# Optimization experiments

Measured on AMD Instinct MI355X. Metric: run time of the kernel, lower is better.

## Reference

```python
import jax, jax.numpy as jnp
import numpy as np

B, C, H, W = 16, 128, 64, 64
C_OUT = 256
N_BANDS = 4
KS = [3, 5, 7, 11]
BN_EPS = 1e-5


def setup_inputs() -> dict:
    key = jax.random.key(0)
    ks = jax.random.split(key, 16)
    inp = {
        'x': jax.random.normal(ks[0], (B, C, H, W), dtype=jnp.float32),
        'conv_w0': jax.random.normal(ks[1], (C, 1, 3), dtype=jnp.float32) * 0.2,
        'conv_w1': jax.random.normal(ks[2], (C, 1, 5), dtype=jnp.float32) * 0.2,
        'conv_w2': jax.random.normal(ks[3], (C, 1, 7), dtype=jnp.float32) * 0.2,
        'conv_w3': jax.random.normal(ks[4], (C, 1, 11), dtype=jnp.float32) * 0.2,
        'bn_gamma': jax.random.uniform(ks[5], (N_BANDS, C), dtype=jnp.float32, minval=0.5, maxval=1.5),
        'bn_beta': jax.random.normal(ks[6], (N_BANDS, C), dtype=jnp.float32) * 0.1,
        'bn_mean': jax.random.normal(ks[7], (N_BANDS, C), dtype=jnp.float32) * 0.1,
        'bn_var': jax.random.uniform(ks[8], (N_BANDS, C), dtype=jnp.float32, minval=0.5, maxval=1.5),
        'scale_weights': jnp.ones((N_BANDS,), dtype=jnp.float32),
        'alpha': jnp.float32(0.5),
        'proj_w': jax.random.normal(ks[9], (C_OUT, C * N_BANDS), dtype=jnp.float32) * 0.04,
        'proj_b': jax.random.normal(ks[10], (C_OUT,), dtype=jnp.float32) * 0.02,
    }
    return inp


def _dwconv1d(xc, w):
    # xc: [B, C, L], w: [C, 1, k] depthwise, 'same' padding for odd k
    k = w.shape[-1]
    return jax.lax.conv_general_dilated(
        xc, w, window_strides=(1,), padding=[(k // 2, k // 2)],
        feature_group_count=xc.shape[1], dimension_numbers=('NCH', 'OIH', 'NCH'))


def _forward(x, conv_w0, conv_w1, conv_w2, conv_w3, bn_gamma, bn_beta, bn_mean,
             bn_var, scale_weights, alpha, proj_w, proj_b):
    b, c, h, w = x.shape
    L = h * w
    xs = x.reshape(b, c, L)                      # [B, C, L] (== x.view.transpose.transpose)
    norm_w = jax.nn.softmax(scale_weights)       # [n_bands]

    # --- multi-scale depthwise conv branch: conv -> BN(eval) -> GELU -> scale ---
    conv_bands = []
    for i, cw in enumerate([conv_w0, conv_w1, conv_w2, conv_w3]):
        y = _dwconv1d(xs, cw)                    # [B, C, L]
        inv = jax.lax.rsqrt(bn_var[i] + BN_EPS)  # [C]
        y = (y - bn_mean[i][:, None]) * (inv * bn_gamma[i])[:, None] + bn_beta[i][:, None]
        y = jax.nn.gelu(y, approximate=False)    # exact erf GELU (torch default)
        conv_bands.append(y.transpose(0, 2, 1) * norm_w[i])  # [B, L, C]

    # --- frequency band branch (interpolate to size L is identity: conv keeps L) ---
    xt = xs.transpose(0, 2, 1)                   # [B, L, C]
    Xf = jnp.fft.rfft(xt, axis=1)                # [B, n_freqs, C]
    n_freqs = L // 2 + 1
    band_size = n_freqs // N_BANDS
    fidx = jnp.arange(n_freqs)
    alpha_s = jax.nn.sigmoid(alpha)
    fused = []
    for i in range(N_BANDS):
        start = i * band_size
        end = (i + 1) * band_size if i < N_BANDS - 1 else n_freqs
        mask = (fidx >= start) & (fidx < end)
        band = jnp.fft.irfft(jnp.where(mask[None, :, None], Xf, 0), n=L, axis=1)
        fused.append(alpha_s * conv_bands[i] + (1.0 - alpha_s) * band)

    cat = jnp.concatenate(fused, axis=-1)        # [B, L, n_bands*C]
    out = cat @ proj_w.T + proj_b                # [B, L, C_out]
    return out.transpose(0, 2, 1).reshape(b, -1, h, w)


def reference(x, conv_w0, conv_w1, conv_w2, conv_w3, bn_gamma, bn_beta, bn_mean,
              bn_var, scale_weights, alpha, proj_w, proj_b):
    return _forward(x, conv_w0, conv_w1, conv_w2, conv_w3, bn_gamma, bn_beta,
                    bn_mean, bn_var, scale_weights, alpha, proj_w, proj_b)
```

## Files before the change

### kernel.cpp

```cpp
#include <hip/hip_runtime.h>
#include <math.h>

constexpr int LEN = 4096;
constexpr int NTHREADS = 512;
constexpr int PELEM = LEN / NTHREADS;
constexpr float INVN = 1.0f / 4096.0f;

typedef __attribute__((ext_vector_type(8))) short bf16x8;
typedef __attribute__((ext_vector_type(4))) float f32x4;

#define APHYS(I) ((I) + ((I) >> 5))
#define TPHYS(I) ((I) + ((I) >> 5))
#define ZOFF 8

__device__ __forceinline__ unsigned short f2bf(float f) {
    unsigned u = __float_as_uint(f);
    unsigned r = (u + 0x7fffu + ((u >> 16) & 1u)) >> 16;
    return (unsigned short)r;
}

__device__ __forceinline__ int digitrev4(int j) {
    int r = 0;
#pragma unroll
    for (int d = 0; d < 6; ++d) { r = (r << 2) | (j & 3); j >>= 2; }
    return r;
}

__device__ __forceinline__ void cmul(float ar, float ai, float br, float bi,
                                     float& cr, float& ci) {
    cr = ar * br - ai * bi;
    ci = ar * bi + ai * br;
}

template <bool CONJ>
__device__ __forceinline__ void loadtw3(const float* __restrict__ twr,
                                        const float* __restrict__ twi, int k1,
                                        float& w1r, float& w1i, float& w2r, float& w2i,
                                        float& w3r, float& w3i) {
    w1r = twr[TPHYS(k1)];
    float s = twi[TPHYS(k1)];
    w1i = CONJ ? -s : s;
    cmul(w1r, w1i, w1r, w1i, w2r, w2i);
    cmul(w1r, w1i, w2r, w2i, w3r, w3i);
}

__device__ void dif_fft(float* __restrict__ ar, float* __restrict__ ai,
                        const float* __restrict__ twr, const float* __restrict__ twi,
                        int tid) {
#pragma unroll
    for (int s = 5; s >= 0; --s) {
        __syncthreads();
        const int qshift = 2 * s;
        const int quarter = 1 << qshift;
        const int tshift = 2 * (5 - s);
#pragma unroll
        for (int u = 0; u < 1024 / NTHREADS; ++u) {
            int t = tid + NTHREADS * u;
            int j = t & (quarter - 1);
            int g = t >> qshift;
            int base = (g << (qshift + 2)) + j;
            int i0 = APHYS(base), i1 = APHYS(base + quarter),
                i2 = APHYS(base + 2 * quarter), i3 = APHYS(base + 3 * quarter);
            float x0r = ar[i0], x0i = ai[i0];
            float x1r = ar[i1], x1i = ai[i1];
            float x2r = ar[i2], x2i = ai[i2];
            float x3r = ar[i3], x3i = ai[i3];
            float t0r = x0r + x2r, t0i = x0i + x2i;
            float t1r = x0r - x2r, t1i = x0i - x2i;
            float t2r = x1r + x3r, t2i = x1i + x3i;
            float t3r = x1r - x3r, t3i = x1i - x3i;
            float y0r = t0r + t2r, y0i = t0i + t2i;
            float y2r = t0r - t2r, y2i = t0i - t2i;
            float y1r = t1r + t3i, y1i = t1i - t3r;
            float y3r = t1r - t3i, y3i = t1i + t3r;
            int k1 = j << tshift;
            float w1r, w1i, w2r, w2i, w3r, w3i;
            loadtw3<false>(twr, twi, k1, w1r, w1i, w2r, w2i, w3r, w3i);
            ar[i0] = y0r;                         ai[i0] = y0i;
            ar[i1] = y1r * w1r - y1i * w1i;       ai[i1] = y1r * w1i + y1i * w1r;
            ar[i2] = y2r * w2r - y2i * w2i;       ai[i2] = y2r * w2i + y2i * w2r;
            ar[i3] = y3r * w3r - y3i * w3i;       ai[i3] = y3r * w3i + y3i * w3r;
        }
    }
    __syncthreads();
}

__device__ void dit_ifft(float* __restrict__ ar, float* __restrict__ ai,
                         const float* __restrict__ twr, const float* __restrict__ twi,
                         int tid) {
#pragma unroll
    for (int s = 0; s <= 5; ++s) {
        __syncthreads();
        const int qshift = 2 * s;
        const int quarter = 1 << qshift;
        const int tshift = 2 * (5 - s);
#pragma unroll
        for (int u = 0; u < 1024 / NTHREADS; ++u) {
            int t = tid + NTHREADS * u;
            int j = t & (quarter - 1);
            int g = t >> qshift;
            int base = (g << (qshift + 2)) + j;
            int i0 = APHYS(base), i1 = APHYS(base + quarter),
                i2 = APHYS(base + 2 * quarter), i3 = APHYS(base + 3 * quarter);
            int k1 = j << tshift;
            float w1r, w1i, w2r, w2i, w3r, w3i;
            loadtw3<true>(twr, twi, k1, w1r, w1i, w2r, w2i, w3r, w3i);
            float x0r = ar[i0], x0i = ai[i0];
            float b1r = ar[i1], b1i = ai[i1];
            float b2r = ar[i2], b2i = ai[i2];
            float b3r = ar[i3], b3i = ai[i3];
            float x1r = b1r * w1r - b1i * w1i, x1i = b1r * w1i + b1i * w1r;
            float x2r = b2r * w2r - b2i * w2i, x2i = b2r * w2i + b2i * w2r;
            float x3r = b3r * w3r - b3i * w3i, x3i = b3r * w3i + b3i * w3r;
            float t0r = x0r + x2r, t0i = x0i + x2i;
            float t1r = x0r - x2r, t1i = x0i - x2i;
            float t2r = x1r + x3r, t2i = x1i + x3i;
            float t3r = x1r - x3r, t3i = x1i - x3i;
            float y0r = t0r + t2r, y0i = t0i + t2i;
            float y2r = t0r - t2r, y2i = t0i - t2i;
            float y1r = t1r - t3i, y1i = t1i + t3r;
            float y3r = t1r + t3i, y3i = t1i - t3r;
            ar[i0] = y0r; ai[i0] = y0i;
            ar[i1] = y1r; ai[i1] = y1i;
            ar[i2] = y2r; ai[i2] = y2i;
            ar[i3] = y3r; ai[i3] = y3i;
        }
    }
    __syncthreads();
}

__global__ __launch_bounds__(512) void k_bands(
    const float* __restrict__ x,
    const float* __restrict__ cw0, const float* __restrict__ cw1,
    const float* __restrict__ cw2, const float* __restrict__ cw3,
    const float* __restrict__ bng, const float* __restrict__ bnb,
    const float* __restrict__ bnm, const float* __restrict__ bnv,
    const float* __restrict__ sw, const float* __restrict__ alp,
    unsigned int* __restrict__ Fu) {
    __shared__ float zr[LEN + 16], zi[LEN + 16];
    __shared__ float wr[4224], wi[4224];
    __shared__ float twr[1056], twi[1056];

    const int tid = threadIdx.x;
    const int pair = blockIdx.x;
    const int b = blockIdx.y;
    const int c0 = 2 * pair, c1 = c0 + 1;

    const float* xp0 = x + ((size_t)b * 128 + c0) * LEN;
    const float* xp1 = xp0 + LEN;
#pragma unroll
    for (int p = 0; p < PELEM; ++p) {
        int l = tid + NTHREADS * p;
        float a0 = xp0[l], a1 = xp1[l];
        zr[ZOFF + l] = a0; zi[ZOFF + l] = a1;
        wr[APHYS(l)] = a0; wi[APHYS(l)] = a1;
    }
    if (tid < 8) {
        zr[tid] = 0.f; zi[tid] = 0.f;
        zr[ZOFF + LEN + tid] = 0.f; zi[ZOFF + LEN + tid] = 0.f;
    }
    for (int jj = tid; jj < 1024; jj += NTHREADS) {
        float ang = -(float)(2.0 * M_PI / 4096.0) * (float)jj;
        float sv, cv;
        sincosf(ang, &sv, &cv);
        twr[TPHYS(jj)] = cv; twi[TPHYS(jj)] = sv;
    }
    dif_fft(wr, wi, twr, twi, tid);

    float Zre[PELEM], Zim[PELEM];
#pragma unroll
    for (int p = 0; p < PELEM; ++p) {
        int l = tid + NTHREADS * p;
        Zre[p] = wr[APHYS(l)]; Zim[p] = wi[APHYS(l)];
    }

    float s0w = sw[0], s1w = sw[1], s2w = sw[2], s3w = sw[3];
    float mx = fmaxf(fmaxf(s0w, s1w), fmaxf(s2w, s3w));
    float e0 = expf(s0w - mx), e1 = expf(s1w - mx), e2 = expf(s2w - mx), e3 = expf(s3w - mx);
    float esum = e0 + e1 + e2 + e3;
    float nwv[4] = {e0 / esum, e1 / esum, e2 / esum, e3 / esum};
    float alpha_s = 1.0f / (1.0f + expf(-alp[0]));
    float oma = 1.0f - alpha_s;

    const float* cwp[4] = {cw0, cw1, cw2, cw3};
    const int kk4[4] = {3, 5, 7, 11};

    float accr[PELEM], acci[PELEM];
#pragma unroll
    for (int p = 0; p < PELEM; ++p) { accr[p] = 0.f; acci[p] = 0.f; }

    unsigned int* dst = Fu + (size_t)b * (512 * LEN / 2);
    const int n = tid & 15;

#pragma unroll
    for (int band = 0; band < 4; ++band) {
        if (band < 3) {
            const int fs = band * 512, fe = fs + 512;
#pragma unroll
            for (int p = 0; p < PELEM; ++p) {
                int j = tid + NTHREADS * p;
                int f = digitrev4(j);
                int fi = (f <= 2048) ? f : (4096 - f);
                bool keep = (fi >= fs) && (fi < fe);
                wr[APHYS(j)] = keep ? Zre[p] : 0.0f;
                wi[APHYS(j)] = keep ? Zim[p] : 0.0f;
            }
            dit_ifft(wr, wi, twr, twi, tid);
        }

        const float* cw = cwp[band];
        const int kk = kk4[band];
        const int kh = kk >> 1;
        float w0c[11], w1c[11];
        for (int q = 0; q < kk; ++q) {
            w0c[q] = cw[c0 * kk + q];
            w1c[q] = cw[c1 * kk + q];
        }
        float A0 = rsqrtf(bnv[band * 128 + c0] + 1e-5f) * bng[band * 128 + c0];
        float B0 = bnb[band * 128 + c0] - bnm[band * 128 + c0] * A0;
        float A1 = rsqrtf(bnv[band * 128 + c1] + 1e-5f) * bng[band * 128 + c1];
        float B1 = bnb[band * 128 + c1] - bnm[band * 128 + c1] * A1;
        float nww = nwv[band];
#pragma unroll
        for (int p = 0; p < PELEM; ++p) {
            int l = tid + NTHREADS * p;
            float bvr, bvi;
            if (band < 3) {
                bvr = wr[APHYS(l)] * INVN;
                bvi = wi[APHYS(l)] * INVN;
                accr[p] += bvr;
                acci[p] += bvi;
            } else {
                bvr = zr[ZOFF + l] - accr[p];
                bvi = zi[ZOFF + l] - acci[p];
            }
            float s0 = 0.f, s1 = 0.f;
#pragma unroll
            for (int q = 0; q < 11; ++q) {
                if (q < kk) {
                    int idx = ZOFF + l + q - kh;
                    s0 += zr[idx] * w0c[q];
                    s1 += zi[idx] * w1c[q];
                }
            }
            float y0 = s0 * A0 + B0;
            y0 = 0.5f * y0 * (1.0f + erff(y0 * 0.70710678118654752f)) * nww;
            float y1 = s1 * A1 + B1;
            y1 = 0.5f * y1 * (1.0f + erff(y1 * 0.70710678118654752f)) * nww;
            float f0 = alpha_s * y0 + oma * bvr;
            float f1 = alpha_s * y1 + oma * bvi;
            int lb = (tid >> 4) + 32 * p;
            unsigned int val = (unsigned int)f2bf(f0) | ((unsigned int)f2bf(f1) << 16);
            dst[((lb * 64 + pair) * 16 + n) * 4 + band] = val;
        }
    }
}

__global__ void k_prep(const float* __restrict__ pw, unsigned short* __restrict__ Wq) {
    int idx = blockIdx.x * 256 + threadIdx.x;
    int o = idx >> 9, c = idx & 511;
    int band = c >> 7, pair = (c & 127) >> 1, lo = c & 1;
    int dstidx = (((o >> 4) * 64 + pair) * 16 + (o & 15)) * 8 + 2 * band + lo;
    Wq[dstidx] = f2bf(pw[idx]);
}

__global__ __launch_bounds__(256) void k_gemm(
    const unsigned short* __restrict__ Wq, const unsigned short* __restrict__ Fq,
    const float* __restrict__ pb, float* __restrict__ out) {
    const int tid = threadIdx.x;
    const int wave = tid >> 6, lane = tid & 63;
    const int h = lane >> 4, n16 = lane & 15;
    const int lt = blockIdx.x, b = blockIdx.y;
    const unsigned short* Fb = Fq + (size_t)b * 2097152;

    f32x4 acc[4][4];
#pragma unroll
    for (int mi = 0; mi < 4; ++mi)
#pragma unroll
        for (int ni = 0; ni < 4; ++ni) acc[mi][ni] = (f32x4){0.f, 0.f, 0.f, 0.f};

#pragma unroll
    for (int ks = 0; ks < 16; ++ks) {
        bf16x8 af[4], bfr[4];
#pragma unroll
        for (int mi = 0; mi < 4; ++mi) {
            int mb = wave * 4 + mi;
            af[mi] = *(const bf16x8*)(Wq + ((((mb * 64) + 4 * ks + h) * 16 + n16) << 3));
        }
#pragma unroll
        for (int ni = 0; ni < 4; ++ni) {
            int lb = lt * 4 + ni;
            bfr[ni] = *(const bf16x8*)(Fb + ((((lb * 64) + 4 * ks + h) * 16 + n16) << 3));
        }
#pragma unroll
        for (int mi = 0; mi < 4; ++mi)
#pragma unroll
            for (int ni = 0; ni < 4; ++ni)
                acc[mi][ni] = __builtin_amdgcn_mfma_f32_16x16x32_bf16(
                    af[mi], bfr[ni], acc[mi][ni], 0, 0, 0);
    }

#pragma unroll
    for (int mi = 0; mi < 4; ++mi) {
#pragma unroll
        for (int r = 0; r < 4; ++r) {
            int o = wave * 64 + mi * 16 + h * 4 + r;
            float bias = pb[o];
#pragma unroll
            for (int ni = 0; ni < 4; ++ni) {
                int l = lt * 64 + ni * 16 + n16;
                out[((size_t)(b * 256 + o)) * LEN + l] = acc[mi][ni][r] + bias;
            }
        }
    }
}

extern "C" void kernel_launch(void* const* d_in, const int* in_sizes, int n_in,
                              void* d_out, int out_size, void* d_ws, size_t ws_size,
                              hipStream_t stream) {
    const float* x   = (const float*)d_in[0];
    const float* cw0 = (const float*)d_in[1];
    const float* cw1 = (const float*)d_in[2];
    const float* cw2 = (const float*)d_in[3];
    const float* cw3 = (const float*)d_in[4];
    const float* bng = (const float*)d_in[5];
    const float* bnb = (const float*)d_in[6];
    const float* bnm = (const float*)d_in[7];
    const float* bnv = (const float*)d_in[8];
    const float* sw  = (const float*)d_in[9];
    const float* alp = (const float*)d_in[10];
    const float* pw  = (const float*)d_in[11];
    const float* pb  = (const float*)d_in[12];
    float* out = (float*)d_out;

    unsigned short* Wq = (unsigned short*)d_ws;
    unsigned int* Fu = (unsigned int*)((char*)d_ws + 262144);

    k_prep<<<512, 256, 0, stream>>>(pw, Wq);

    const size_t perB = (size_t)512 * LEN * 2;
    int chunk = (int)((ws_size > 262144 ? ws_size - 262144 : 0) / perB);
    if (chunk < 1) chunk = 1;
    if (chunk > 16) chunk = 16;

    for (int b0 = 0; b0 < 16; b0 += chunk) {
        int nb = 16 - b0 < chunk ? 16 - b0 : chunk;
        dim3 g1(64, nb);
        k_bands<<<g1, NTHREADS, 0, stream>>>(
            x + (size_t)b0 * 128 * LEN, cw0, cw1, cw2, cw3,
            bng, bnb, bnm, bnv, sw, alp, Fu);
        dim3 g2(64, nb);
        k_gemm<<<g2, 256, 0, stream>>>(
            Wq, (const unsigned short*)Fu, pb, out + (size_t)b0 * 256 * LEN);
    }
}
```

Measured before the change: 159.0 us.

## Shrink k_bands shared memory to raise occupancy via packed bf16 input and half twiddle table

Cuts the shared-memory footprint of the band kernel so more blocks fit per CU. The raw input is stored as packed bf16 pairs instead of two fp32 arrays, and the twiddle table is halved by deriving the upper half through a 45-degree rotation. The padding stride is reduced and the launch bounds request 6 waves per EU. In exchange, the depthwise conv now reads bf16-rounded inputs, which costs accuracy, and it adds bounds checks and extra twiddle arithmetic. The last band re-reads x from global memory.

New measurement: 280.9 us. 76.7% more time.

```diff
diff --git a/kernel.cpp b/kernel.cpp
--- a/kernel.cpp
+++ b/kernel.cpp
@@ -5,13 +5,13 @@
 constexpr int NTHREADS = 512;
 constexpr int PELEM = LEN / NTHREADS;
 constexpr float INVN = 1.0f / 4096.0f;
+constexpr float RHALF = 0.70710678118654752440f;
 
 typedef __attribute__((ext_vector_type(8))) short bf16x8;
 typedef __attribute__((ext_vector_type(4))) float f32x4;
 
-#define APHYS(I) ((I) + ((I) >> 5))
-#define TPHYS(I) ((I) + ((I) >> 5))
-#define ZOFF 8
+#define APHYS(I) ((I) + ((I) >> 6))
+#define TPHYS(I) ((I) + ((I) >> 6))
 
 __device__ __forceinline__ unsigned short f2bf(float f) {
     unsigned u = __float_as_uint(f);
@@ -37,9 +37,14 @@
                                         const float* __restrict__ twi, int k1,
                                         float& w1r, float& w1i, float& w2r, float& w2i,
                                         float& w3r, float& w3i) {
-    w1r = twr[TPHYS(k1)];
-    float s = twi[TPHYS(k1)];
-    w1i = CONJ ? -s : s;
+    int m = k1 & 511;
+    float a = twr[TPHYS(m)];
+    float s = twi[TPHYS(m)];
+    bool hi = (k1 & 512) != 0;
+    float r = hi ? RHALF * (a + s) : a;
+    float im = hi ? RHALF * (s - a) : s;
+    w1r = r;
+    w1i = CONJ ? -im : im;
     cmul(w1r, w1i, w1r, w1i, w2r, w2i);
     cmul(w1r, w1i, w2r, w2i, w3r, w3i);
 }
@@ -129,7 +134,7 @@
     __syncthreads();
 }
 
-__global__ __launch_bounds__(512) void k_bands(
+__global__ __launch_bounds__(512, 6) void k_bands(
     const float* __restrict__ x,
     const float* __restrict__ cw0, const float* __restrict__ cw1,
     const float* __restrict__ cw2, const float* __restrict__ cw3,
@@ -137,9 +142,9 @@
     const float* __restrict__ bnm, const float* __restrict__ bnv,
     const float* __restrict__ sw, const float* __restrict__ alp,
     unsigned int* __restrict__ Fu) {
-    __shared__ float zr[LEN + 16], zi[LEN + 16];
-    __shared__ float wr[4224], wi[4224];
-    __shared__ float twr[1056], twi[1056];
+    __shared__ float wr[4160], wi[4160];
+    __shared__ float twr[520], twi[520];
+    __shared__ unsigned zpk[LEN];
 
     const int tid = threadIdx.x;
     const int pair = blockIdx.x;
@@ -152,14 +157,11 @@
     for (int p = 0; p < PELEM; ++p) {
         int l = tid + NTHREADS * p;
         float a0 = xp0[l], a1 = xp1[l];
-        zr[ZOFF + l] = a0; zi[ZOFF + l] = a1;
+        zpk[l] = (unsigned)f2bf(a0) | ((unsigned)f2bf(a1) << 16);
         wr[APHYS(l)] = a0; wi[APHYS(l)] = a1;
     }
-    if (tid < 8) {
-        zr[tid] = 0.f; zi[tid] = 0.f;
-        zr[ZOFF + LEN + tid] = 0.f; zi[ZOFF + LEN + tid] = 0.f;
-    }
-    for (int jj = tid; jj < 1024; jj += NTHREADS) {
+    if (tid < 512) {
+        int jj = tid;
         float ang = -(float)(2.0 * M_PI / 4096.0) * (float)jj;
         float sv, cv;
         sincosf(ang, &sv, &cv);
@@ -211,11 +213,6 @@
         const float* cw = cwp[band];
         const int kk = kk4[band];
         const int kh = kk >> 1;
-        float w0c[11], w1c[11];
-        for (int q = 0; q < kk; ++q) {
-            w0c[q] = cw[c0 * kk + q];
-            w1c[q] = cw[c1 * kk + q];
-        }
         float A0 = rsqrtf(bnv[band * 128 + c0] + 1e-5f) * bng[band * 128 + c0];
         float B0 = bnb[band * 128 + c0] - bnm[band * 128 + c0] * A0;
         float A1 = rsqrtf(bnv[band * 128 + c1] + 1e-5f) * bng[band * 128 + c1];
@@ -231,22 +228,27 @@
                 accr[p] += bvr;
                 acci[p] += bvi;
             } else {
-                bvr = zr[ZOFF + l] - accr[p];
-                bvi = zi[ZOFF + l] - acci[p];
+                bvr = xp0[l] - accr[p];
+                bvi = xp1[l] - acci[p];
             }
             float s0 = 0.f, s1 = 0.f;
 #pragma unroll
             for (int q = 0; q < 11; ++q) {
                 if (q < kk) {
-                    int idx = ZOFF + l + q - kh;
-                    s0 += zr[idx] * w0c[q];
-                    s1 += zi[idx] * w1c[q];
+                    int idx = l + q - kh;
+                    bool ok = (idx >= 0) && (idx < LEN);
+                    int ic = idx < 0 ? 0 : (idx > LEN - 1 ? LEN - 1 : idx);
+                    unsigned uv = zpk[ic];
+                    float v0 = ok ? __uint_as_float(uv << 16) : 0.0f;
+                    float v1 = ok ? __uint_as_float(uv & 0xffff0000u) : 0.0f;
+                    s0 += v0 * cw[c0 * kk + q];
+                    s1 += v1 * cw[c1 * kk + q];
                 }
             }
             float y0 = s0 * A0 + B0;
-            y0 = 0.5f * y0 * (1.0f + erff(y0 * 0.70710678118654752f)) * nww;
+            y0 = 0.5f * y0 * (1.0f + erff(y0 * RHALF)) * nww;
             float y1 = s1 * A1 + B1;
-            y1 = 0.5f * y1 * (1.0f + erff(y1 * 0.70710678118654752f)) * nww;
+            y1 = 0.5f * y1 * (1.0f + erff(y1 * RHALF)) * nww;
             float f0 = alpha_s * y0 + oma * bvr;
             float f1 = alpha_s * y1 + oma * bvi;
             int lb = (tid >> 4) + 32 * p;
```

## Switch 4096-point FFT/IFFT from radix-4 to radix-8 stages

Applied to the files above, without the earlier changes.

Replaces the six-stage radix-4 DIF FFT and DIT IFFT with four-stage radix-8 versions. Each thread now handles one 8-point butterfly per stage, so there are fewer barriers and fewer shared-memory round trips per transform, and the twiddle table shrinks to 512 entries. The bit-reversal for band masking changes to octal digit reversal. The trade-off is more registers per thread and twiddle powers computed by chained complex multiplies, which may add rounding error.

Measured after the change: 142.3 us. 1.12x faster.

```diff
diff --git a/kernel.cpp b/kernel.cpp
--- a/kernel.cpp
+++ b/kernel.cpp
@@ -5,6 +5,7 @@
 constexpr int NTHREADS = 512;
 constexpr int PELEM = LEN / NTHREADS;
 constexpr float INVN = 1.0f / 4096.0f;
+constexpr float RHALF = 0.70710678118654752440f;
 
 typedef __attribute__((ext_vector_type(8))) short bf16x8;
 typedef __attribute__((ext_vector_type(4))) float f32x4;
@@ -19,11 +20,8 @@
     return (unsigned short)r;
 }
 
-__device__ __forceinline__ int digitrev4(int j) {
-    int r = 0;
-#pragma unroll
-    for (int d = 0; d < 6; ++d) { r = (r << 2) | (j & 3); j >>= 2; }
-    return r;
+__device__ __forceinline__ int digitrev8(int j) {
+    return ((j & 7) << 9) | (((j >> 3) & 7) << 6) | (((j >> 6) & 7) << 3) | (j >> 9);
 }
 
 __device__ __forceinline__ void cmul(float ar, float ai, float br, float bi,
@@ -32,98 +30,149 @@
     ci = ar * bi + ai * br;
 }
 
-template <bool CONJ>
-__device__ __forceinline__ void loadtw3(const float* __restrict__ twr,
-                                        const float* __restrict__ twi, int k1,
-                                        float& w1r, float& w1i, float& w2r, float& w2i,
-                                        float& w3r, float& w3i) {
-    w1r = twr[TPHYS(k1)];
-    float s = twi[TPHYS(k1)];
-    w1i = CONJ ? -s : s;
-    cmul(w1r, w1i, w1r, w1i, w2r, w2i);
-    cmul(w1r, w1i, w2r, w2i, w3r, w3i);
-}
-
-__device__ void dif_fft(float* __restrict__ ar, float* __restrict__ ai,
-                        const float* __restrict__ twr, const float* __restrict__ twi,
-                        int tid) {
-#pragma unroll
-    for (int s = 5; s >= 0; --s) {
-        __syncthreads();
-        const int qshift = 2 * s;
-        const int quarter = 1 << qshift;
-        const int tshift = 2 * (5 - s);
-#pragma unroll
-        for (int u = 0; u < 1024 / NTHREADS; ++u) {
-            int t = tid + NTHREADS * u;
-            int j = t & (quarter - 1);
-            int g = t >> qshift;
-            int base = (g << (qshift + 2)) + j;
-            int i0 = APHYS(base), i1 = APHYS(base + quarter),
-                i2 = APHYS(base + 2 * quarter), i3 = APHYS(base + 3 * quarter);
-            float x0r = ar[i0], x0i = ai[i0];
-            float x1r = ar[i1], x1i = ai[i1];
-            float x2r = ar[i2], x2i = ai[i2];
-            float x3r = ar[i3], x3i = ai[i3];
-            float t0r = x0r + x2r, t0i = x0i + x2i;
-            float t1r = x0r - x2r, t1i = x0i - x2i;
-            float t2r = x1r + x3r, t2i = x1i + x3i;
-            float t3r = x1r - x3r, t3i = x1i - x3i;
-            float y0r = t0r + t2r, y0i = t0i + t2i;
-            float y2r = t0r - t2r, y2i = t0i - t2i;
-            float y1r = t1r + t3i, y1i = t1i - t3r;
-            float y3r = t1r - t3i, y3i = t1i + t3r;
-            int k1 = j << tshift;
-            float w1r, w1i, w2r, w2i, w3r, w3i;
-            loadtw3<false>(twr, twi, k1, w1r, w1i, w2r, w2i, w3r, w3i);
-            ar[i0] = y0r;                         ai[i0] = y0i;
-            ar[i1] = y1r * w1r - y1i * w1i;       ai[i1] = y1r * w1i + y1i * w1r;
-            ar[i2] = y2r * w2r - y2i * w2i;       ai[i2] = y2r * w2i + y2i * w2r;
-            ar[i3] = y3r * w3r - y3i * w3i;       ai[i3] = y3r * w3i + y3i * w3r;
-        }
-    }
-    __syncthreads();
-}
-
-__device__ void dit_ifft(float* __restrict__ ar, float* __restrict__ ai,
+__device__ void dif_fft8(float* __restrict__ ar, float* __restrict__ ai,
                          const float* __restrict__ twr, const float* __restrict__ twi,
                          int tid) {
 #pragma unroll
-    for (int s = 0; s <= 5; ++s) {
+    for (int s = 0; s < 4; ++s) {
         __syncthreads();
-        const int qshift = 2 * s;
-        const int quarter = 1 << qshift;
-        const int tshift = 2 * (5 - s);
-#pragma unroll
-        for (int u = 0; u < 1024 / NTHREADS; ++u) {
-            int t = tid + NTHREADS * u;
-            int j = t & (quarter - 1);
-            int g = t >> qshift;
-            int base = (g << (qshift + 2)) + j;
-            int i0 = APHYS(base), i1 = APHYS(base + quarter),
-                i2 = APHYS(base + 2 * quarter), i3 = APHYS(base + 3 * quarter);
-            int k1 = j << tshift;
-            float w1r, w1i, w2r, w2i, w3r, w3i;
-            loadtw3<true>(twr, twi, k1, w1r, w1i, w2r, w2i, w3r, w3i);
-            float x0r = ar[i0], x0i = ai[i0];
-            float b1r = ar[i1], b1i = ai[i1];
-            float b2r = ar[i2], b2i = ai[i2];
-            float b3r = ar[i3], b3i = ai[i3];
-            float x1r = b1r * w1r - b1i * w1i, x1i = b1r * w1i + b1i * w1r;
-            float x2r = b2r * w2r - b2i * w2i, x2i = b2r * w2i + b2i * w2r;
-            float x3r = b3r * w3r - b3i * w3i, x3i = b3r * w3i + b3i * w3r;
-            float t0r = x0r + x2r, t0i = x0i + x2i;
-            float t1r = x0r - x2r, t1i = x0i - x2i;
-            float t2r = x1r + x3r, t2i = x1i + x3i;
-            float t3r = x1r - x3r, t3i = x1i - x3i;
-            float y0r = t0r + t2r, y0i = t0i + t2i;
-            float y2r = t0r - t2r, y2i = t0i - t2i;
-            float y1r = t1r - t3i, y1i = t1i + t3r;
-            float y3r = t1r + t3i, y3i = t1i - t3r;
-            ar[i0] = y0r; ai[i0] = y0i;
-            ar[i1] = y1r; ai[i1] = y1i;
-            ar[i2] = y2r; ai[i2] = y2i;
-            ar[i3] = y3r; ai[i3] = y3i;
+        const int eshift = 3 * (3 - s);
+        const int E = 1 << eshift;
+        int j = tid & (E - 1);
+        int g = tid >> eshift;
+        int base = (g << (eshift + 3)) + j;
+
+        float xr[8], xi[8];
+#pragma unroll
+        for (int m = 0; m < 8; ++m) {
+            int idx = APHYS(base + (m << eshift));
+            xr[m] = ar[idx]; xi[m] = ai[idx];
+        }
+        float b0r = xr[0] + xr[4], b0i = xi[0] + xi[4];
+        float b1r = xr[1] + xr[5], b1i = xi[1] + xi[5];
+        float b2r = xr[2] + xr[6], b2i = xi[2] + xi[6];
+        float b3r = xr[3] + xr[7], b3i = xi[3] + xi[7];
+        float c0r = xr[0] - xr[4], c0i = xi[0] - xi[4];
+        float c1r = xr[1] - xr[5], c1i = xi[1] - xi[5];
+        float c2r = xr[2] - xr[6], c2i = xi[2] - xi[6];
+        float c3r = xr[3] - xr[7], c3i = xi[3] - xi[7];
+        float d1r = RHALF * (c1r + c1i), d1i = RHALF * (c1i - c1r);
+        float d2r = c2i,               d2i = -c2r;
+        float d3r = -RHALF * (c3r - c3i), d3i = -RHALF * (c3r + c3i);
+        float t0r = b0r + b2r, t0i = b0i + b2i;
+        float t1r = b0r - b2r, t1i = b0i - b2i;
+        float t2r = b1r + b3r, t2i = b1i + b3i;
+        float t3r = b1r - b3r, t3i = b1i - b3i;
+        xr[0] = t0r + t2r; xi[0] = t0i + t2i;
+        xr[2] = t1r + t3i; xi[2] = t1i - t3r;
+        xr[4] = t0r - t2r; xi[4] = t0i - t2i;
+        xr[6] = t1r - t3i; xi[6] = t1i + t3r;
+        t0r = c0r + d2r; t0i = c0i + d2i;
+        t1r = c0r - d2r; t1i = c0i - d2i;
+        t2r = d1r + d3r; t2i = d1i + d3i;
+        t3r = d1r - d3r; t3i = d1i - d3i;
+        xr[1] = t0r + t2r; xi[1] = t0i + t2i;
+        xr[3] = t1r + t3i; xi[3] = t1i - t3r;
+        xr[5] = t0r - t2r; xi[5] = t0i - t2i;
+        xr[7] = t1r - t3i; xi[7] = t1i + t3r;
+
+        if (s < 3) {
+            int k1 = j << (3 * s);
+            float w1r = twr[TPHYS(k1)], w1i = twi[TPHYS(k1)];
+            float w2r, w2i, w3r, w3i, w4r, w4i, w5r, w5i, w6r, w6i, w7r, w7i;
+            cmul(w1r, w1i, w1r, w1i, w2r, w2i);
+            cmul(w2r, w2i, w1r, w1i, w3r, w3i);
+            cmul(w2r, w2i, w2r, w2i, w4r, w4i);
+            cmul(w4r, w4i, w1r, w1i, w5r, w5i);
+            cmul(w4r, w4i, w2r, w2i, w6r, w6i);
+            cmul(w4r, w4i, w3r, w3i, w7r, w7i);
+            float orr, oii;
+            cmul(xr[1], xi[1], w1r, w1i, orr, oii); xr[1] = orr; xi[1] = oii;
+            cmul(xr[2], xi[2], w2r, w2i, orr, oii); xr[2] = orr; xi[2] = oii;
+            cmul(xr[3], xi[3], w3r, w3i, orr, oii); xr[3] = orr; xi[3] = oii;
+            cmul(xr[4], xi[4], w4r, w4i, orr, oii); xr[4] = orr; xi[4] = oii;
+            cmul(xr[5], xi[5], w5r, w5i, orr, oii); xr[5] = orr; xi[5] = oii;
+            cmul(xr[6], xi[6], w6r, w6i, orr, oii); xr[6] = orr; xi[6] = oii;
+            cmul(xr[7], xi[7], w7r, w7i, orr, oii); xr[7] = orr; xi[7] = oii;
+        }
+#pragma unroll
+        for (int m = 0; m < 8; ++m) {
+            int idx = APHYS(base + (m << eshift));
+            ar[idx] = xr[m]; ai[idx] = xi[m];
+        }
+    }
+    __syncthreads();
+}
+
+__device__ void dit_ifft8(float* __restrict__ ar, float* __restrict__ ai,
+                          const float* __restrict__ twr, const float* __restrict__ twi,
+                          int tid) {
+#pragma unroll
+    for (int s = 0; s < 4; ++s) {
+        __syncthreads();
+        const int eshift = 3 * s;
+        const int E = 1 << eshift;
+        int j = tid & (E - 1);
+        int g = tid >> eshift;
+        int base = (g << (eshift + 3)) + j;
+
+        float xr[8], xi[8];
+#pragma unroll
+        for (int m = 0; m < 8; ++m) {
+            int idx = APHYS(base + (m << eshift));
+            xr[m] = ar[idx]; xi[m] = ai[idx];
+        }
+        if (s > 0) {
+            int k1 = j << (3 * (3 - s));
+            float w1r = twr[TPHYS(k1)], w1i = -twi[TPHYS(k1)];
+            float w2r, w2i, w3r, w3i, w4r, w4i, w5r, w5i, w6r, w6i, w7r, w7i;
+            cmul(w1r, w1i, w1r, w1i, w2r, w2i);
+            cmul(w2r, w2i, w1r, w1i, w3r, w3i);
+            cmul(w2r, w2i, w2r, w2i, w4r, w4i);
+            cmul(w4r, w4i, w1r, w1i, w5r, w5i);
+            cmul(w4r, w4i, w2r, w2i, w6r, w6i);
+            cmul(w4r, w4i, w3r, w3i, w7r, w7i);
+            float orr, oii;
+            cmul(xr[1], xi[1], w1r, w1i, orr, oii); xr[1] = orr; xi[1] = oii;
+            cmul(xr[2], xi[2], w2r, w2i, orr, oii); xr[2] = orr; xi[2] = oii;
+            cmul(xr[3], xi[3], w3r, w3i, orr, oii); xr[3] = orr; xi[3] = oii;
+            cmul(xr[4], xi[4], w4r, w4i, orr, oii); xr[4] = orr; xi[4] = oii;
+            cmul(xr[5], xi[5], w5r, w5i, orr, oii); xr[5] = orr; xi[5] = oii;
+            cmul(xr[6], xi[6], w6r, w6i, orr, oii); xr[6] = orr; xi[6] = oii;
+            cmul(xr[7], xi[7], w7r, w7i, orr, oii); xr[7] = orr; xi[7] = oii;
+        }
+        float b0r = xr[0] + xr[4], b0i = xi[0] + xi[4];
+        float b1r = xr[1] + xr[5], b1i = xi[1] + xi[5];
+        float b2r = xr[2] + xr[6], b2i = xi[2] + xi[6];
+        float b3r = xr[3] + xr[7], b3i = xi[3] + xi[7];
+        float c0r = xr[0] - xr[4], c0i = xi[0] - xi[4];
+        float c1r = xr[1] - xr[5], c1i = xi[1] - xi[5];
+        float c2r = xr[2] - xr[6], c2i = xi[2] - xi[6];
+        float c3r = xr[3] - xr[7], c3i = xi[3] - xi[7];
+        float d1r = RHALF * (c1r - c1i), d1i = RHALF * (c1r + c1i);
+        float d2r = -c2i,              d2i = c2r;
+        float d3r = -RHALF * (c3r + c3i), d3i = RHALF * (c3r - c3i);
+        float t0r = b0r + b2r, t0i = b0i + b2i;
+        float t1r = b0r - b2r, t1i = b0i - b2i;
+        float t2r = b1r + b3r, t2i = b1i + b3i;
+        float t3r = b1r - b3r, t3i = b1i - b3i;
+        xr[0] = t0r + t2r; xi[0] = t0i + t2i;
+        xr[2] = t1r - t3i; xi[2] = t1i + t3r;
+        xr[4] = t0r - t2r; xi[4] = t0i - t2i;
+        xr[6] = t1r + t3i; xi[6] = t1i - t3r;
+        t0r = c0r + d2r; t0i = c0i + d2i;
+        t1r = c0r - d2r; t1i = c0i - d2i;
+        t2r = d1r + d3r; t2i = d1i + d3i;
+        t3r = d1r - d3r; t3i = d1i - d3i;
+        xr[1] = t0r + t2r; xi[1] = t0i + t2i;
+        xr[3] = t1r - t3i; xi[3] = t1i + t3r;
+        xr[5] = t0r - t2r; xi[5] = t0i - t2i;
+        xr[7] = t1r + t3i; xi[7] = t1i - t3r;
+
+#pragma unroll
+        for (int m = 0; m < 8; ++m) {
+            int idx = APHYS(base + (m << eshift));
+            ar[idx] = xr[m]; ai[idx] = xi[m];
         }
     }
     __syncthreads();
@@ -139,7 +188,7 @@
     unsigned int* __restrict__ Fu) {
     __shared__ float zr[LEN + 16], zi[LEN + 16];
     __shared__ float wr[4224], wi[4224];
-    __shared__ float twr[1056], twi[1056];
+    __shared__ float twr[528], twi[528];
 
     const int tid = threadIdx.x;
     const int pair = blockIdx.x;
@@ -159,13 +208,14 @@
         zr[tid] = 0.f; zi[tid] = 0.f;
         zr[ZOFF + LEN + tid] = 0.f; zi[ZOFF + LEN + tid] = 0.f;
     }
-    for (int jj = tid; jj < 1024; jj += NTHREADS) {
+    {
+        int jj = tid;
         float ang = -(float)(2.0 * M_PI / 4096.0) * (float)jj;
         float sv, cv;
         sincosf(ang, &sv, &cv);
         twr[TPHYS(jj)] = cv; twi[TPHYS(jj)] = sv;
     }
-    dif_fft(wr, wi, twr, twi, tid);
+    dif_fft8(wr, wi, twr, twi, tid);
 
     float Zre[PELEM], Zim[PELEM];
 #pragma unroll
@@ -199,13 +249,13 @@
 #pragma unroll
             for (int p = 0; p < PELEM; ++p) {
                 int j = tid + NTHREADS * p;
-                int f = digitrev4(j);
+                int f = digitrev8(j);
                 int fi = (f <= 2048) ? f : (4096 - f);
                 bool keep = (fi >= fs) && (fi < fe);
                 wr[APHYS(j)] = keep ? Zre[p] : 0.0f;
                 wi[APHYS(j)] = keep ? Zim[p] : 0.0f;
             }
-            dit_ifft(wr, wi, twr, twi, tid);
+            dit_ifft8(wr, wi, twr, twi, tid);
         }
 
         const float* cw = cwp[band];
@@ -244,9 +294,9 @@
                 }
             }
             float y0 = s0 * A0 + B0;
-            y0 = 0.5f * y0 * (1.0f + erff(y0 * 0.70710678118654752f)) * nww;
+            y0 = 0.5f * y0 * (1.0f + erff(y0 * RHALF)) * nww;
             float y1 = s1 * A1 + B1;
-            y1 = 0.5f * y1 * (1.0f + erff(y1 * 0.70710678118654752f)) * nww;
+            y1 = 0.5f * y1 * (1.0f + erff(y1 * RHALF)) * nww;
             float f0 = alpha_s * y0 + oma * bvr;
             float f1 = alpha_s * y1 + oma * bvi;
             int lb = (tid >> 4) + 32 * p;
```
